# Performance work log

Measured on AMD Instinct MI355X. Metric: run time of the kernel, lower is better.

The kernel has to match this reference:

```python
import jax, jax.numpy as jnp
import numpy as np

ALPHA = 0.2          # LeakyReLU negative slope
ORTHO_LAMBDA = 0.01  # orthogonal regularization weight


def setup_inputs() -> dict:
    key = jax.random.key(0)
    ks = jax.random.split(key, 9)
    N, IN, OUT, NR, H = 50000, 128, 128, 64, 4
    E1, E2 = 200000, 50000
    return {
        "input": jax.random.normal(ks[0], (N, IN), jnp.float32),
        "edge": jax.random.randint(ks[1], (2, E1), 0, N),
        "edge_embed": jax.random.normal(ks[2], (E1, NR), jnp.float32),
        "edge_list_nhop": jax.random.randint(ks[3], (2, E2), 0, N),
        "edge_embed_nhop": jax.random.normal(ks[4], (E2, NR), jnp.float32),
        "proj": jax.random.normal(ks[5], (H, IN, IN), jnp.float32) / np.sqrt(IN).astype(np.float32),
        "W": jax.random.normal(ks[6], (H, OUT, 2 * IN + NR), jnp.float32) * 0.08,
        "a": jax.random.normal(ks[7], (H, 1, OUT), jnp.float32) * 0.1,
        "head_weights": jnp.ones((H,), jnp.float32),
    }


def reference(input, edge, edge_embed, edge_list_nhop, edge_embed_nhop, proj, W, a, head_weights):
    N, IN = input.shape
    H, OUT, _ = W.shape
    e = jnp.concatenate([edge, edge_list_nhop], axis=1)              # [2, E]
    emb = jnp.concatenate([edge_embed, edge_embed_nhop], axis=0)     # [E, NR]
    src, tgt = e[0], e[1]

    # per-head orthogonal projections: head_input[h] = input @ proj[h].T -> [H, N, IN]
    hin = jnp.einsum('ni,hoi->hno', input, proj)

    # edge_m = W @ concat(h_src, h_tgt, rel) without materializing the concat
    W_src, W_tgt, W_rel = W[:, :, :IN], W[:, :, IN:2 * IN], W[:, :, 2 * IN:]
    edge_m = (jnp.einsum('hei,hoi->heo', hin[:, src, :], W_src)
              + jnp.einsum('hei,hoi->heo', hin[:, tgt, :], W_tgt)
              + jnp.einsum('er,hor->heo', emb, W_rel))               # [H, E, OUT]

    scores = jnp.einsum('heo,ho->he', edge_m, a[:, 0, :])            # [H, E]
    powers = -jnp.where(scores > 0, scores, ALPHA * scores)         # -leakyrelu
    edge_e = jnp.exp(powers)                                         # [H, E]

    seg = lambda v: jax.ops.segment_sum(v, src, num_segments=N)
    e_rowsum = jnp.clip(jax.vmap(seg)(edge_e), 1e-12, None)          # [H, N]

    edge_w = edge_e[:, :, None] * edge_m                             # [H, E, OUT]
    head_out = jax.vmap(seg)(edge_w)                                 # [H, N, OUT]

    w = jax.nn.softmax(head_weights)
    out = jnp.einsum('h,hnd->nd', w, head_out)                       # [N, OUT]
    # faithful to torch: divides by the LAST head's e_rowsum (loop leakage)
    out = out / e_rowsum[-1][:, None]

    pp = jnp.einsum('hij,hkj->hik', proj, proj)                      # proj @ proj.T
    eye = jnp.eye(proj.shape[1], dtype=proj.dtype)
    orth_reg = ORTHO_LAMBDA * jnp.sum(jnp.sqrt(jnp.sum((pp - eye) ** 2, axis=(1, 2))))

    return jax.nn.elu(out), orth_reg
```

## Files before the change

### kernel.cpp

```cpp
#include <hip/hip_runtime.h>
#include <math.h>


#define NHEAD 4

typedef unsigned short u16;
typedef __attribute__((ext_vector_type(4))) unsigned short u16x4;
typedef __attribute__((ext_vector_type(8))) unsigned short u16x8;
typedef __attribute__((ext_vector_type(8))) short bf16x8;
typedef __attribute__((ext_vector_type(4))) float f32x4;

__device__ __forceinline__ float bf2f(u16 v) {
    union { unsigned u; float f; } x; x.u = ((unsigned)v) << 16; return x.f;
}
__device__ __forceinline__ u16 f2bf(float f) {
    union { float f; unsigned u; } x; x.f = f;
    const unsigned r = x.u + 0x7FFFu + ((x.u >> 16) & 1u);
    return (u16)(r >> 16);
}

__global__ __launch_bounds__(256) void k1_prep(
    const float* __restrict__ proj, const float* __restrict__ W,
    const float* __restrict__ a, const float* __restrict__ hw,
    u16* __restrict__ M_bf,
    float* __restrict__ asrc, float* __restrict__ atgt, float* __restrict__ arel,
    u16* __restrict__ WcatT_bf, float* __restrict__ wsoft,
    float* __restrict__ orth_part)
{
    __shared__ float projS[128*132];
    __shared__ float WS[32*132];
    __shared__ float tS[128];
    __shared__ float red[256];
    const int h = blockIdx.x;
    const int part = blockIdx.y;
    const int z = blockIdx.z;
    const int tid = threadIdx.x;
    if (part < 2 && z >= 4) return;
    const float* projH = proj + h*(128*128);
    const float* WH = W + h*(128*320);
    const float* aH = a + h*128;

    {
        const float4* p4 = (const float4*)projH;
        for (int idx = tid; idx < 4096; idx += 256)
            *(float4*)&projS[(idx>>5)*132 + (idx&31)*4] = p4[idx];
    }

    if (part < 2) {
        const int koff = part ? 128 : 0;
        for (int idx = tid; idx < 1024; idx += 256) {
            const int ol = idx>>5, jq = idx&31;
            *(float4*)&WS[ol*132 + jq*4] = *(const float4*)&WH[(z*32+ol)*320 + koff + jq*4];
        }
        __syncthreads();
        u16* Mout = M_bf + ((size_t)(part*4 + h))*16384;
        for (int idx = tid; idx < 1024; idx += 256) {
            const int ol = idx>>5, jq = idx&31;
            float4 acc; acc.x=0.f; acc.y=0.f; acc.z=0.f; acc.w=0.f;
            for (int i = 0; i < 128; ++i) {
                const float wv = WS[ol*132 + i];
                const float4 pv = *(const float4*)&projS[i*132 + jq*4];
                acc.x += wv*pv.x; acc.y += wv*pv.y; acc.z += wv*pv.z; acc.w += wv*pv.w;
            }
            u16x4 pk; pk.x=f2bf(acc.x); pk.y=f2bf(acc.y); pk.z=f2bf(acc.z); pk.w=f2bf(acc.w);
            *(u16x4*)&Mout[(z*32+ol)*128 + jq*4] = pk;
        }
        if (z == 0) {
            if (tid < 128) {
                float s = 0.f;
                for (int o = 0; o < 128; ++o) s += aH[o]*WH[o*320 + koff + tid];
                tS[tid] = s;
            }
            __syncthreads();
            if (tid < 128) {
                float s = 0.f;
                for (int i = 0; i < 128; ++i) s += tS[i]*projS[i*132 + tid];
                (part ? atgt : asrc)[h*128 + tid] = s;
            }
        }
    } else {
        __syncthreads();
        float local = 0.f;
        const int base = z*2048;
        for (int idx = base + tid; idx < base + 2048; idx += 256) {
            const int i = idx>>7, k = idx&127;
            if (i > k) continue;
            float s = 0.f;
            for (int q = 0; q < 32; ++q) {
                const float4 pi = *(const float4*)&projS[i*132 + q*4];
                const float4 pk = *(const float4*)&projS[k*132 + q*4];
                s += pi.x*pk.x + pi.y*pk.y + pi.z*pk.z + pi.w*pk.w;
            }
            if (i == k) { s -= 1.f; local += s*s; }
            else local += 2.f*s*s;
        }
        red[tid] = local;
        __syncthreads();
        for (int st = 128; st > 0; st >>= 1) {
            if (tid < st) red[tid] += red[tid+st];
            __syncthreads();
        }
        if (tid == 0) atomicAdd(&orth_part[h], red[0]);
        if (z == 0) {
            if (tid < 64) {
                float s = 0.f;
                for (int o = 0; o < 128; ++o) s += aH[o]*WH[o*320 + 256 + tid];
                arel[h*64 + tid] = s;
            }
            for (int idx = tid; idx < 8192; idx += 256) {
                const int r = idx & 63, o = idx >> 6;
                WcatT_bf[(size_t)o*256 + h*64 + r] = f2bf(WH[o*320 + 256 + r]);
            }
            if (h == 0 && tid == 0) {
                const float m = fmaxf(fmaxf(hw[0],hw[1]), fmaxf(hw[2],hw[3]));
                const float e0=expf(hw[0]-m), e1=expf(hw[1]-m), e2=expf(hw[2]-m), e3=expf(hw[3]-m);
                const float s = e0+e1+e2+e3;
                wsoft[0]=e0/s; wsoft[1]=e1/s; wsoft[2]=e2/s; wsoft[3]=e3/s;
            }
        }
    }
}

__global__ __launch_bounds__(256) void k0_nodes(
    const float* __restrict__ input, const float* __restrict__ asrc, const float* __restrict__ atgt,
    u16* __restrict__ in_bf, float* __restrict__ s_src, float* __restrict__ s_tgt, int N)
{
    __shared__ float aS[512], tS[512];
    const int tid = threadIdx.x;
    for (int idx = tid; idx < 512; idx += 256) { aS[idx] = asrc[idx]; tS[idx] = atgt[idx]; }
    __syncthreads();
    const int n = blockIdx.x*256 + tid;
    if (n >= N) return;
    const float4* inr = (const float4*)(input + (size_t)n*128);
    u16* ob = in_bf + (size_t)n*128;
    float ss[4] = {0.f,0.f,0.f,0.f}, st[4] = {0.f,0.f,0.f,0.f};
    for (int q = 0; q < 32; ++q) {
        const float4 v = inr[q];
        u16x4 pk; pk.x=f2bf(v.x); pk.y=f2bf(v.y); pk.z=f2bf(v.z); pk.w=f2bf(v.w);
        *(u16x4*)(ob + q*4) = pk;
        #pragma unroll
        for (int hh = 0; hh < 4; ++hh) {
            const float4 av = *(const float4*)&aS[hh*128 + q*4];
            const float4 tv = *(const float4*)&tS[hh*128 + q*4];
            ss[hh] += v.x*av.x + v.y*av.y + v.z*av.z + v.w*av.w;
            st[hh] += v.x*tv.x + v.y*tv.y + v.z*tv.z + v.w*tv.w;
        }
    }
    float4 o1; o1.x=ss[0]; o1.y=ss[1]; o1.z=ss[2]; o1.w=ss[3];
    float4 o2; o2.x=st[0]; o2.y=st[1]; o2.z=st[2]; o2.w=st[3];
    *(float4*)(s_src + (size_t)n*4) = o1;
    *(float4*)(s_tgt + (size_t)n*4) = o2;
}

__global__ __launch_bounds__(256) void k2_mfma(
    const u16* __restrict__ in_bf, const u16* __restrict__ M_bf,
    u16* __restrict__ tbl, int N)
{
    __shared__ u16 MS[16384];
    __shared__ u16 DW[4][16*136];
    const int tid = threadIdx.x;
    const int w = tid >> 6, lane = tid & 63;
    const int bid = blockIdx.x;
    const int nx = gridDim.x >> 3;
    const int swz = (bid & 7)*nx + (bid >> 3);
    const int n0 = (swz >> 3)*256;
    const int mat = swz & 7;
    const int m = lane & 15, kg = lane >> 4;

    {
        const u16* Mp = M_bf + (size_t)mat*16384;
        for (int c = tid; c < 2048; c += 256) {
            const int row = c >> 4, c16 = c & 15;
            const u16x8 v = *(const u16x8*)(Mp + row*128 + c16*8);
            *(u16x8*)((char*)MS + row*256 + ((c16*16) ^ ((row&7)<<4))) = v;
        }
    }
    __syncthreads();

    bf16x8 fa[8][4];
    #pragma unroll
    for (int nt = 0; nt < 8; ++nt) {
        const int row = nt*16 + m;
        #pragma unroll
        for (int ks = 0; ks < 4; ++ks) {
            const int c16 = ks*4 + kg;
            fa[nt][ks] = *(const bf16x8*)((const char*)MS + row*256 + ((c16*16) ^ ((row&7)<<4)));
        }
    }

    for (int sub = 0; sub < 4; ++sub) {
        const int nrow = n0 + w*64 + sub*16 + m;
        const int nclamp = (nrow < N) ? nrow : (N-1);
        bf16x8 fb[4];
        #pragma unroll
        for (int ks = 0; ks < 4; ++ks)
            fb[ks] = *(const bf16x8*)(in_bf + (size_t)nclamp*128 + ks*32 + kg*8);
        f32x4 acc[8];
        #pragma unroll
        for (int nt = 0; nt < 8; ++nt) { acc[nt][0]=0.f; acc[nt][1]=0.f; acc[nt][2]=0.f; acc[nt][3]=0.f; }
        #pragma unroll
        for (int nt = 0; nt < 8; ++nt)
            #pragma unroll
            for (int ks = 0; ks < 4; ++ks)
                acc[nt] = __builtin_amdgcn_mfma_f32_16x16x32_bf16(fa[nt][ks], fb[ks], acc[nt], 0, 0, 0);
        #pragma unroll
        for (int nt = 0; nt < 8; ++nt) {
            unsigned lo, hi;
            asm("v_cvt_pk_bf16_f32 %0, %1, %2" : "=v"(lo) : "v"(acc[nt][0]), "v"(acc[nt][1]));
            asm("v_cvt_pk_bf16_f32 %0, %1, %2" : "=v"(hi) : "v"(acc[nt][2]), "v"(acc[nt][3]));
            uint2 pk; pk.x = lo; pk.y = hi;
            *(uint2*)&DW[w][m*136 + nt*16 + kg*4] = pk;
        }
        __syncthreads();
        const int nb = n0 + w*64 + sub*16;
        #pragma unroll
        for (int k = 0; k < 4; ++k) {
            const int idx = lane + k*64;
            const int row = idx >> 4, seg = idx & 15;
            const int n = nb + row;
            if (n < N) {
                const bf16x8 v = *(const bf16x8*)&DW[w][row*136 + seg*8];
                *(bf16x8*)(tbl + (size_t)n*1024 + mat*128 + seg*8) = v;
            }
        }
        __syncthreads();
    }
}

__global__ __launch_bounds__(256) void k_deg(
    const int* __restrict__ edge, const int* __restrict__ nhop,
    int* __restrict__ deg, int E1, int E2)
{
    const int e = blockIdx.x*256 + threadIdx.x;
    if (e >= E1+E2) return;
    const int src = (e < E1) ? edge[e] : nhop[e-E1];
    atomicAdd(&deg[src], 1);
}

__global__ __launch_bounds__(1024) void k_scanA(const int* __restrict__ deg, int* __restrict__ offsets,
                                                int* __restrict__ bsum, int N)
{
    __shared__ int wsumS[16];
    const int tid = threadIdx.x;
    const int lane = tid & 63, wid = tid >> 6;
    const int i0 = blockIdx.x*4096 + tid*4;
    int a0=0,a1=0,a2=0,a3=0;
    if (i0 + 3 < N) { const int4 t = *(const int4*)(deg + i0); a0=t.x; a1=t.y; a2=t.z; a3=t.w; }
    else { if (i0 < N) a0=deg[i0]; if (i0+1 < N) a1=deg[i0+1]; if (i0+2 < N) a2=deg[i0+2]; }
    const int s1=a0+a1, s2=s1+a2, s3=s2+a3;
    int s = s3;
    #pragma unroll
    for (int d = 1; d < 64; d <<= 1) { const int t = __shfl_up(s, d); if (lane >= d) s += t; }
    if (lane == 63) wsumS[wid] = s;
    __syncthreads();
    if (tid < 16) {
        int t = wsumS[tid];
        #pragma unroll
        for (int d = 1; d < 16; d <<= 1) { const int u = __shfl_up(t, d); if (tid >= d) t += u; }
        wsumS[tid] = t;
    }
    __syncthreads();
    const int ex = (wid ? wsumS[wid-1] : 0) + s - s3;
    if (i0 < N)     offsets[i0]   = ex;
    if (i0+1 < N)   offsets[i0+1] = ex + a0;
    if (i0+2 < N)   offsets[i0+2] = ex + s1;
    if (i0+3 < N)   offsets[i0+3] = ex + s2;
    if (tid == 0) bsum[blockIdx.x] = wsumS[15];
}

__global__ __launch_bounds__(64) void k_scanB(const int* __restrict__ bsum, int* __restrict__ boff,
                                              int* __restrict__ offsets, int nb, int N)
{
    const int tid = threadIdx.x;
    const int v = (tid < nb) ? bsum[tid] : 0;
    int s = v;
    #pragma unroll
    for (int d = 1; d < 64; d <<= 1) { const int t = __shfl_up(s, d); if (tid >= d) s += t; }
    if (tid < nb) boff[tid] = s - v;
    if (tid == 63) offsets[N] = s;
}

__global__ __launch_bounds__(256) void k_fill2(
    const int* __restrict__ edge, const int* __restrict__ nhop,
    const float* __restrict__ emb1, const float* __restrict__ emb2,
    const float* __restrict__ s_src, const float* __restrict__ s_tgt,
    const float* __restrict__ arel,
    const int* __restrict__ offsets, const int* __restrict__ boff, int* __restrict__ cursor,
    int* __restrict__ csr_tgt, float* __restrict__ ee_perm, u16* __restrict__ emb_perm,
    int E1, int E2)
{
    const int tid = threadIdx.x;
    const int g = tid >> 4, l = tid & 15;
    const int E = E1 + E2;
    const float4 ar0 = *(const float4*)(arel + 0*64 + l*4);
    const float4 ar1 = *(const float4*)(arel + 1*64 + l*4);
    const float4 ar2 = *(const float4*)(arel + 2*64 + l*4);
    const float4 ar3 = *(const float4*)(arel + 3*64 + l*4);
    const int ebase = blockIdx.x*256;
    #pragma unroll 4
    for (int it = 0; it < 16; ++it) {
        const int e = ebase + it*16 + g;
        if (e >= E) continue;
        const float4 v = (e < E1) ? *(const float4*)(emb1 + (size_t)e*64 + l*4)
                                  : *(const float4*)(emb2 + (size_t)(e-E1)*64 + l*4);
        u16x4 pk; pk.x=f2bf(v.x); pk.y=f2bf(v.y); pk.z=f2bf(v.z); pk.w=f2bf(v.w);
        float p0 = v.x*ar0.x + v.y*ar0.y + v.z*ar0.z + v.w*ar0.w;
        float p1 = v.x*ar1.x + v.y*ar1.y + v.z*ar1.z + v.w*ar1.w;
        float p2 = v.x*ar2.x + v.y*ar2.y + v.z*ar2.z + v.w*ar2.w;
        float p3 = v.x*ar3.x + v.y*ar3.y + v.z*ar3.z + v.w*ar3.w;
        #pragma unroll
        for (int d = 1; d < 16; d <<= 1) {
            p0 += __shfl_xor(p0, d);
            p1 += __shfl_xor(p1, d);
            p2 += __shfl_xor(p2, d);
            p3 += __shfl_xor(p3, d);
        }
        int p = 0;
        if (l == 0) {
            int src, tgt;
            if (e < E1) { src = edge[e]; tgt = edge[E1+e]; }
            else { const int e2 = e-E1; src = nhop[e2]; tgt = nhop[E2+e2]; }
            const float4 s4 = *(const float4*)(s_src + (size_t)src*4);
            const float4 t4 = *(const float4*)(s_tgt + (size_t)tgt*4);
            float4 eo;
            { const float sc = s4.x+t4.x+p0; eo.x = expf(sc>0.f ? -sc : -0.2f*sc); }
            { const float sc = s4.y+t4.y+p1; eo.y = expf(sc>0.f ? -sc : -0.2f*sc); }
            { const float sc = s4.z+t4.z+p2; eo.z = expf(sc>0.f ? -sc : -0.2f*sc); }
            { const float sc = s4.w+t4.w+p3; eo.w = expf(sc>0.f ? -sc : -0.2f*sc); }
            const int pos = atomicAdd(&cursor[src], 1);
            p = offsets[src] + boff[src>>12] + pos;
            csr_tgt[p] = tgt;
            *(float4*)(ee_perm + (size_t)p*4) = eo;
        }
        p = __shfl(p, tid & 48);
        *(u16x4*)(emb_perm + (size_t)p*64 + l*4) = pk;
    }
}

__global__ __launch_bounds__(256) void k4_gather(
    const float* __restrict__ ee_perm, const int* __restrict__ offsets, const int* __restrict__ boff,
    const int* __restrict__ csr_tgt,
    const u16* __restrict__ emb_perm, const u16* __restrict__ tbl,
    const float* __restrict__ wsoft,
    u16* __restrict__ pout_bf, u16* __restrict__ semb_bf, float* __restrict__ rowsum3,
    int N)
{
    __shared__ float eeS[4][64][4];
    __shared__ int   tgS[4][64];
    const int lane = threadIdx.x & 63;
    const int wv = threadIdx.x >> 6;
    const int n = blockIdx.x*4 + wv;
    if (n >= N) return;
    const int hl = lane >> 4;
    const int hoff = hl*128 + (lane & 15)*8;

    union HT { u16x8 v; unsigned u[4]; };

    float acc[8];
    #pragma unroll
    for (int j = 0; j < 8; ++j) acc[j] = 0.f;
    float sm0=0.f, sm1=0.f, sm2=0.f, sm3=0.f;
    float rsl0=0.f, rsl1=0.f, rsl2=0.f, rsl3=0.f;

    const int start = offsets[n] + boff[n>>12];
    const int end = (n+1 == N) ? offsets[N] : (offsets[n+1] + boff[(n+1)>>12]);
    for (int cb = start; cb < end; cb += 64) {
        const int rem = end - cb;
        const int cnt = rem < 64 ? rem : 64;
        int tgtL = 0;
        float4 eeL; eeL.x=0.f; eeL.y=0.f; eeL.z=0.f; eeL.w=0.f;
        if (lane < cnt) {
            tgtL = csr_tgt[cb + lane];
            eeL  = *(const float4*)(ee_perm + (size_t)(cb + lane)*4);
        }
        rsl0 += eeL.x; rsl1 += eeL.y; rsl2 += eeL.z; rsl3 += eeL.w;
        *(float4*)&eeS[wv][lane][0] = eeL;
        tgS[wv][lane] = tgtL;
        const int cp = (cnt + 3) & ~3;

        HT zz; zz.u[0]=0u; zz.u[1]=0u; zz.u[2]=0u; zz.u[3]=0u;
        HT ht0=zz, ht1=zz, ht2=zz, ht3=zz;
        u16 em0=0, em1=0, em2=0, em3=0;
#define K4_FETCH(J, IDX) { const int tg_ = tgS[wv][IDX]; \
            ht##J.v = *(const u16x8*)(tbl + (size_t)tg_*1024 + 512 + hoff); \
            em##J = emb_perm[(size_t)(cb + (IDX))*64 + lane]; }
        if (0 < cnt) K4_FETCH(0, 0)
        if (1 < cnt) K4_FETCH(1, 1)
        if (2 < cnt) K4_FETCH(2, 2)
        if (3 < cnt) K4_FETCH(3, 3)

#define K4_STAGE(J) { \
            const float4 ee4 = *(const float4*)&eeS[wv][i+J][0]; \
            const float eh = eeS[wv][i+J][hl]; \
            _Pragma("unroll") \
            for (int p = 0; p < 4; ++p) { \
                union{unsigned u; float f;} lo_, hi_; \
                lo_.u = ht##J.u[p] << 16; hi_.u = ht##J.u[p] & 0xffff0000u; \
                acc[2*p]   += eh*lo_.f; \
                acc[2*p+1] += eh*hi_.f; \
            } \
            const float ev = bf2f(em##J); \
            sm0 += ee4.x*ev; sm1 += ee4.y*ev; sm2 += ee4.z*ev; sm3 += ee4.w*ev; \
            { const int ii = i + 4 + J; if (ii < cnt) K4_FETCH(J, ii) } }

        for (int i = 0; i < cp; i += 4) {
            K4_STAGE(0)
            K4_STAGE(1)
            K4_STAGE(2)
            K4_STAGE(3)
        }
#undef K4_STAGE
#undef K4_FETCH
    }

    #pragma unroll
    for (int d = 1; d < 64; d <<= 1) {
        rsl0 += __shfl_xor(rsl0, d);
        rsl1 += __shfl_xor(rsl1, d);
        rsl2 += __shfl_xor(rsl2, d);
        rsl3 += __shfl_xor(rsl3, d);
    }
    {
        const float rsh = (hl==0)?rsl0:(hl==1)?rsl1:(hl==2)?rsl2:rsl3;
        HT hs; hs.v = *(const u16x8*)(tbl + (size_t)n*1024 + hoff);
        #pragma unroll
        for (int p = 0; p < 4; ++p) {
            union{unsigned u; float f;} lo_, hi_;
            lo_.u = hs.u[p] << 16; hi_.u = hs.u[p] & 0xffff0000u;
            acc[2*p]   += rsh*lo_.f;
            acc[2*p+1] += rsh*hi_.f;
        }
    }
    if (lane == 0) rowsum3[n] = fmaxf(rsl3, 1e-12f);

    const float4 ws4 = *(const float4*)wsoft;
    const float wh = (hl==0)?ws4.x:(hl==1)?ws4.y:(hl==2)?ws4.z:ws4.w;
    float p[8];
    #pragma unroll
    for (int j = 0; j < 8; ++j) {
        float pv = wh*acc[j];
        pv += __shfl_xor(pv, 16);
        pv += __shfl_xor(pv, 32);
        p[j] = pv;
    }
    if (hl == 0) {
        u16 pk[8];
        #pragma unroll
        for (int j = 0; j < 8; ++j) pk[j] = f2bf(p[j]);
        *(u16x8*)(pout_bf + (size_t)n*128 + (lane & 15)*8) = *(u16x8*)pk;
    }
    u16* so = semb_bf + (size_t)n*256;
    so[lane]       = f2bf(ws4.x*sm0);
    so[64 + lane]  = f2bf(ws4.y*sm1);
    so[128 + lane] = f2bf(ws4.z*sm2);
    so[192 + lane] = f2bf(ws4.w*sm3);
}

__global__ __launch_bounds__(256) void k5_gemm(
    const u16* __restrict__ semb_bf, const u16* __restrict__ wcatT_bf,
    const u16* __restrict__ pout_bf,
    const float* __restrict__ rowsum3, const float* __restrict__ orth_part,
    float* __restrict__ out, int N)
{
    __shared__ float DS[64*132];
    const int tid = threadIdx.x;
    if (blockIdx.x == 0 && tid == 0)
        out[(size_t)N*128] = 0.01f*(sqrtf(orth_part[0])+sqrtf(orth_part[1])+sqrtf(orth_part[2])+sqrtf(orth_part[3]));
    const int w = tid >> 6, lane = tid & 63;
    const int m = lane & 15, kg = lane >> 4;
    const int n0 = blockIdx.x*64;

    bf16x8 fa[8];
    {
        int row = n0 + w*16 + m; if (row >= N) row = N-1;
        const u16* ap = semb_bf + (size_t)row*256 + kg*8;
        #pragma unroll
        for (int ks = 0; ks < 8; ++ks) fa[ks] = *(const bf16x8*)(ap + ks*32);
    }
    f32x4 acc[8];
    #pragma unroll
    for (int nt = 0; nt < 8; ++nt) { acc[nt][0]=0.f; acc[nt][1]=0.f; acc[nt][2]=0.f; acc[nt][3]=0.f; }
    #pragma unroll
    for (int nt = 0; nt < 8; ++nt) {
        const u16* bp = wcatT_bf + (size_t)(nt*16 + m)*256 + kg*8;
        #pragma unroll
        for (int ks = 0; ks < 8; ++ks) {
            const bf16x8 fb = *(const bf16x8*)(bp + ks*32);
            acc[nt] = __builtin_amdgcn_mfma_f32_16x16x32_bf16(fa[ks], fb, acc[nt], 0, 0, 0);
        }
    }
    #pragma unroll
    for (int nt = 0; nt < 8; ++nt) {
        const int o = nt*16 + m;
        const int r0 = w*16 + kg*4;
        #pragma unroll
        for (int r = 0; r < 4; ++r)
            DS[(r0+r)*132 + o] = acc[nt][r];
    }
    __syncthreads();
    for (int idx = tid; idx < 2048; idx += 256) {
        const int row = idx >> 5, q = idx & 31;
        const int n = n0 + row;
        if (n < N) {
            const float4 d = *(const float4*)&DS[row*132 + q*4];
            const u16x4 pb = *(const u16x4*)(pout_bf + (size_t)n*128 + q*4);
            const float rinv = 1.0f / rowsum3[n];
            float v0 = (bf2f(pb.x) + d.x)*rinv;
            float v1 = (bf2f(pb.y) + d.y)*rinv;
            float v2 = (bf2f(pb.z) + d.z)*rinv;
            float v3 = (bf2f(pb.w) + d.w)*rinv;
            v0 = (v0 > 0.f) ? v0 : expm1f(v0);
            v1 = (v1 > 0.f) ? v1 : expm1f(v1);
            v2 = (v2 > 0.f) ? v2 : expm1f(v2);
            v3 = (v3 > 0.f) ? v3 : expm1f(v3);
            float4 r4; r4.x=v0; r4.y=v1; r4.z=v2; r4.w=v3;
            *(float4*)(out + (size_t)n*128 + q*4) = r4;
        }
    }
}

extern "C" void kernel_launch(void* const* d_in, const int* in_sizes, int n_in,
                              void* d_out, int out_size, void* d_ws, size_t ws_size,
                              hipStream_t stream)
{
    const float* input = (const float*)d_in[0];
    const int*   edge  = (const int*)d_in[1];
    const float* emb1  = (const float*)d_in[2];
    const int*   nhop  = (const int*)d_in[3];
    const float* emb2  = (const float*)d_in[4];
    const float* proj  = (const float*)d_in[5];
    const float* W     = (const float*)d_in[6];
    const float* a     = (const float*)d_in[7];
    const float* hw    = (const float*)d_in[8];
    float* out = (float*)d_out;

    const int N  = in_sizes[0] / 128;
    const int E1 = in_sizes[1] / 2;
    const int E2 = in_sizes[3] / 2;
    const int E  = E1 + E2;
    (void)n_in; (void)out_size; (void)ws_size;

    char* wsb = (char*)d_ws;
    size_t off = 0;
    auto alloc = [&](size_t bytes) -> char* {
        char* p = wsb + off;
        off += (bytes + 255) & ~(size_t)255;
        return p;
    };
    u16*   in_bf    = (u16*)alloc((size_t)N*128*2);
    u16*   tbl      = (u16*)alloc((size_t)N*1024*2);
    u16*   semb_bf  = (u16*)alloc((size_t)N*256*2);
    u16*   pout_bf  = (u16*)alloc((size_t)N*128*2);
    u16*   emb_perm = (u16*)alloc((size_t)E*64*2);
    float* ee_perm  = (float*)alloc((size_t)E*4*4);
    int*   csr_tgt  = (int*)alloc((size_t)E*4);
    u16*   M_bf     = (u16*)alloc((size_t)8*16384*2);
    u16*   WcatT_bf = (u16*)alloc((size_t)128*256*2);
    float* asrc     = (float*)alloc(512*4);
    float* atgt     = (float*)alloc(512*4);
    float* arel     = (float*)alloc(256*4);
    float* s_src    = (float*)alloc((size_t)N*4*4);
    float* s_tgt    = (float*)alloc((size_t)N*4*4);
    float* wsoft    = (float*)alloc(4*4);
    float* rowsum3  = (float*)alloc((size_t)N*4);
    int*   offsets  = (int*)alloc((size_t)(N+1)*4);
    int*   bsum     = (int*)alloc(64*4);
    int*   boff     = (int*)alloc(64*4);
    const size_t zoff0 = off;
    float* orth_part= (float*)alloc(4*4);
    int*   deg      = (int*)alloc((size_t)N*4);
    int*   cursor   = (int*)alloc((size_t)N*4);
    const size_t zoff1 = off;

    hipMemsetAsync(wsb + zoff0, 0, zoff1 - zoff0, stream);

    const int nbScan = (N + 4095) / 4096;
    const int nx = (N + 255) / 256;

    k1_prep<<<dim3(NHEAD,3,8), dim3(256), 0, stream>>>(proj, W, a, hw, M_bf,
                                                       asrc, atgt, arel, WcatT_bf, wsoft, orth_part);
    k0_nodes<<<dim3((N+255)/256), dim3(256), 0, stream>>>(input, asrc, atgt, in_bf, s_src, s_tgt, N);
    k2_mfma<<<dim3(nx*8), dim3(256), 0, stream>>>(in_bf, M_bf, tbl, N);
    k_deg<<<dim3((E+255)/256), dim3(256), 0, stream>>>(edge, nhop, deg, E1, E2);
    k_scanA<<<dim3(nbScan), dim3(1024), 0, stream>>>(deg, offsets, bsum, N);
    k_scanB<<<dim3(1), dim3(64), 0, stream>>>(bsum, boff, offsets, nbScan, N);
    k_fill2<<<dim3((E+255)/256), dim3(256), 0, stream>>>(edge, nhop, emb1, emb2, s_src, s_tgt,
                                                         arel, offsets, boff, cursor,
                                                         csr_tgt, ee_perm, emb_perm, E1, E2);
    k4_gather<<<dim3((N+3)/4), dim3(256), 0, stream>>>(ee_perm, offsets, boff, csr_tgt, emb_perm,
                                                       tbl, wsoft, pout_bf, semb_bf, rowsum3, N);
    k5_gemm<<<dim3((N+63)/64), dim3(256), 0, stream>>>(semb_bf, WcatT_bf, pout_bf, rowsum3, orth_part,
                                                       out, N);
}
```

Measured before the change: 257.6 us.

## Fuse degree count into node prep and co-schedule edge fill with MFMA table GEMM

Moves the per-edge degree atomics into the node-prep kernel, extending its grid to cover all edges. Merges the edge-fill kernel and the projection-table MFMA kernel into one launch whose blocks branch by index, so the independent fill and GEMM work can overlap. It also removes the block barriers around the per-wave staging buffer in the GEMM path. This cuts launches and idle tails, at the cost of the fill blocks now carrying the GEMM's large shared-memory allocation, which may lower their occupancy.

```diff
diff --git a/kernel.cpp b/kernel.cpp
--- a/kernel.cpp
+++ b/kernel.cpp
@@ -123,13 +123,20 @@
 
 __global__ __launch_bounds__(256) void k0_nodes(
     const float* __restrict__ input, const float* __restrict__ asrc, const float* __restrict__ atgt,
-    u16* __restrict__ in_bf, float* __restrict__ s_src, float* __restrict__ s_tgt, int N)
+    const int* __restrict__ edge, const int* __restrict__ nhop,
+    u16* __restrict__ in_bf, float* __restrict__ s_src, float* __restrict__ s_tgt,
+    int* __restrict__ deg, int N, int E1, int E2)
 {
     __shared__ float aS[512], tS[512];
     const int tid = threadIdx.x;
     for (int idx = tid; idx < 512; idx += 256) { aS[idx] = asrc[idx]; tS[idx] = atgt[idx]; }
+    const int t = blockIdx.x*256 + tid;
+    if (t < E1 + E2) {
+        const int src = (t < E1) ? edge[t] : nhop[t-E1];
+        atomicAdd(&deg[src], 1);
+    }
     __syncthreads();
-    const int n = blockIdx.x*256 + tid;
+    const int n = t;
     if (n >= N) return;
     const float4* inr = (const float4*)(input + (size_t)n*128);
     u16* ob = in_bf + (size_t)n*128;
@@ -150,91 +157,6 @@
     float4 o2; o2.x=st[0]; o2.y=st[1]; o2.z=st[2]; o2.w=st[3];
     *(float4*)(s_src + (size_t)n*4) = o1;
     *(float4*)(s_tgt + (size_t)n*4) = o2;
-}
-
-__global__ __launch_bounds__(256) void k2_mfma(
-    const u16* __restrict__ in_bf, const u16* __restrict__ M_bf,
-    u16* __restrict__ tbl, int N)
-{
-    __shared__ u16 MS[16384];
-    __shared__ u16 DW[4][16*136];
-    const int tid = threadIdx.x;
-    const int w = tid >> 6, lane = tid & 63;
-    const int bid = blockIdx.x;
-    const int nx = gridDim.x >> 3;
-    const int swz = (bid & 7)*nx + (bid >> 3);
-    const int n0 = (swz >> 3)*256;
-    const int mat = swz & 7;
-    const int m = lane & 15, kg = lane >> 4;
-
-    {
-        const u16* Mp = M_bf + (size_t)mat*16384;
-        for (int c = tid; c < 2048; c += 256) {
-            const int row = c >> 4, c16 = c & 15;
-            const u16x8 v = *(const u16x8*)(Mp + row*128 + c16*8);
-            *(u16x8*)((char*)MS + row*256 + ((c16*16) ^ ((row&7)<<4))) = v;
-        }
-    }
-    __syncthreads();
-
-    bf16x8 fa[8][4];
-    #pragma unroll
-    for (int nt = 0; nt < 8; ++nt) {
-        const int row = nt*16 + m;
-        #pragma unroll
-        for (int ks = 0; ks < 4; ++ks) {
-            const int c16 = ks*4 + kg;
-            fa[nt][ks] = *(const bf16x8*)((const char*)MS + row*256 + ((c16*16) ^ ((row&7)<<4)));
-        }
-    }
-
-    for (int sub = 0; sub < 4; ++sub) {
-        const int nrow = n0 + w*64 + sub*16 + m;
-        const int nclamp = (nrow < N) ? nrow : (N-1);
-        bf16x8 fb[4];
-        #pragma unroll
-        for (int ks = 0; ks < 4; ++ks)
-            fb[ks] = *(const bf16x8*)(in_bf + (size_t)nclamp*128 + ks*32 + kg*8);
-        f32x4 acc[8];
-        #pragma unroll
-        for (int nt = 0; nt < 8; ++nt) { acc[nt][0]=0.f; acc[nt][1]=0.f; acc[nt][2]=0.f; acc[nt][3]=0.f; }
-        #pragma unroll
-        for (int nt = 0; nt < 8; ++nt)
-            #pragma unroll
-            for (int ks = 0; ks < 4; ++ks)
-                acc[nt] = __builtin_amdgcn_mfma_f32_16x16x32_bf16(fa[nt][ks], fb[ks], acc[nt], 0, 0, 0);
-        #pragma unroll
-        for (int nt = 0; nt < 8; ++nt) {
-            unsigned lo, hi;
-            asm("v_cvt_pk_bf16_f32 %0, %1, %2" : "=v"(lo) : "v"(acc[nt][0]), "v"(acc[nt][1]));
-            asm("v_cvt_pk_bf16_f32 %0, %1, %2" : "=v"(hi) : "v"(acc[nt][2]), "v"(acc[nt][3]));
-            uint2 pk; pk.x = lo; pk.y = hi;
-            *(uint2*)&DW[w][m*136 + nt*16 + kg*4] = pk;
-        }
-        __syncthreads();
-        const int nb = n0 + w*64 + sub*16;
-        #pragma unroll
-        for (int k = 0; k < 4; ++k) {
-            const int idx = lane + k*64;
-            const int row = idx >> 4, seg = idx & 15;
-            const int n = nb + row;
-            if (n < N) {
-                const bf16x8 v = *(const bf16x8*)&DW[w][row*136 + seg*8];
-                *(bf16x8*)(tbl + (size_t)n*1024 + mat*128 + seg*8) = v;
-            }
-        }
-        __syncthreads();
-    }
-}
-
-__global__ __launch_bounds__(256) void k_deg(
-    const int* __restrict__ edge, const int* __restrict__ nhop,
-    int* __restrict__ deg, int E1, int E2)
-{
-    const int e = blockIdx.x*256 + threadIdx.x;
-    if (e >= E1+E2) return;
-    const int src = (e < E1) ? edge[e] : nhop[e-E1];
-    atomicAdd(&deg[src], 1);
 }
 
 __global__ __launch_bounds__(1024) void k_scanA(const int* __restrict__ deg, int* __restrict__ offsets,
@@ -280,60 +202,133 @@
     if (tid == 63) offsets[N] = s;
 }
 
-__global__ __launch_bounds__(256) void k_fill2(
+__global__ __launch_bounds__(256) void kC_fill_gemm(
     const int* __restrict__ edge, const int* __restrict__ nhop,
     const float* __restrict__ emb1, const float* __restrict__ emb2,
     const float* __restrict__ s_src, const float* __restrict__ s_tgt,
     const float* __restrict__ arel,
     const int* __restrict__ offsets, const int* __restrict__ boff, int* __restrict__ cursor,
     int* __restrict__ csr_tgt, float* __restrict__ ee_perm, u16* __restrict__ emb_perm,
-    int E1, int E2)
-{
+    int E1, int E2, int nfill,
+    const u16* __restrict__ in_bf, const u16* __restrict__ M_bf,
+    u16* __restrict__ tbl, int N, int nx8)
+{
+    __shared__ u16 MS[16384];
+    __shared__ u16 DW[4][16*136];
     const int tid = threadIdx.x;
-    const int g = tid >> 4, l = tid & 15;
-    const int E = E1 + E2;
-    const float4 ar0 = *(const float4*)(arel + 0*64 + l*4);
-    const float4 ar1 = *(const float4*)(arel + 1*64 + l*4);
-    const float4 ar2 = *(const float4*)(arel + 2*64 + l*4);
-    const float4 ar3 = *(const float4*)(arel + 3*64 + l*4);
-    const int ebase = blockIdx.x*256;
-    #pragma unroll 4
-    for (int it = 0; it < 16; ++it) {
-        const int e = ebase + it*16 + g;
-        if (e >= E) continue;
-        const float4 v = (e < E1) ? *(const float4*)(emb1 + (size_t)e*64 + l*4)
-                                  : *(const float4*)(emb2 + (size_t)(e-E1)*64 + l*4);
-        u16x4 pk; pk.x=f2bf(v.x); pk.y=f2bf(v.y); pk.z=f2bf(v.z); pk.w=f2bf(v.w);
-        float p0 = v.x*ar0.x + v.y*ar0.y + v.z*ar0.z + v.w*ar0.w;
-        float p1 = v.x*ar1.x + v.y*ar1.y + v.z*ar1.z + v.w*ar1.w;
-        float p2 = v.x*ar2.x + v.y*ar2.y + v.z*ar2.z + v.w*ar2.w;
-        float p3 = v.x*ar3.x + v.y*ar3.y + v.z*ar3.z + v.w*ar3.w;
-        #pragma unroll
-        for (int d = 1; d < 16; d <<= 1) {
-            p0 += __shfl_xor(p0, d);
-            p1 += __shfl_xor(p1, d);
-            p2 += __shfl_xor(p2, d);
-            p3 += __shfl_xor(p3, d);
-        }
-        int p = 0;
-        if (l == 0) {
-            int src, tgt;
-            if (e < E1) { src = edge[e]; tgt = edge[E1+e]; }
-            else { const int e2 = e-E1; src = nhop[e2]; tgt = nhop[E2+e2]; }
-            const float4 s4 = *(const float4*)(s_src + (size_t)src*4);
-            const float4 t4 = *(const float4*)(s_tgt + (size_t)tgt*4);
-            float4 eo;
-            { const float sc = s4.x+t4.x+p0; eo.x = expf(sc>0.f ? -sc : -0.2f*sc); }
-            { const float sc = s4.y+t4.y+p1; eo.y = expf(sc>0.f ? -sc : -0.2f*sc); }
-            { const float sc = s4.z+t4.z+p2; eo.z = expf(sc>0.f ? -sc : -0.2f*sc); }
-            { const float sc = s4.w+t4.w+p3; eo.w = expf(sc>0.f ? -sc : -0.2f*sc); }
-            const int pos = atomicAdd(&cursor[src], 1);
-            p = offsets[src] + boff[src>>12] + pos;
-            csr_tgt[p] = tgt;
-            *(float4*)(ee_perm + (size_t)p*4) = eo;
-        }
-        p = __shfl(p, tid & 48);
-        *(u16x4*)(emb_perm + (size_t)p*64 + l*4) = pk;
+
+    if (blockIdx.x < nfill) {
+        const int g = tid >> 4, l = tid & 15;
+        const int E = E1 + E2;
+        const float4 ar0 = *(const float4*)(arel + 0*64 + l*4);
+        const float4 ar1 = *(const float4*)(arel + 1*64 + l*4);
+        const float4 ar2 = *(const float4*)(arel + 2*64 + l*4);
+        const float4 ar3 = *(const float4*)(arel + 3*64 + l*4);
+        const int ebase = blockIdx.x*256;
+        #pragma unroll 4
+        for (int it = 0; it < 16; ++it) {
+            const int e = ebase + it*16 + g;
+            if (e >= E) continue;
+            const float4 v = (e < E1) ? *(const float4*)(emb1 + (size_t)e*64 + l*4)
+                                      : *(const float4*)(emb2 + (size_t)(e-E1)*64 + l*4);
+            u16x4 pk; pk.x=f2bf(v.x); pk.y=f2bf(v.y); pk.z=f2bf(v.z); pk.w=f2bf(v.w);
+            float p0 = v.x*ar0.x + v.y*ar0.y + v.z*ar0.z + v.w*ar0.w;
+            float p1 = v.x*ar1.x + v.y*ar1.y + v.z*ar1.z + v.w*ar1.w;
+            float p2 = v.x*ar2.x + v.y*ar2.y + v.z*ar2.z + v.w*ar2.w;
+            float p3 = v.x*ar3.x + v.y*ar3.y + v.z*ar3.z + v.w*ar3.w;
+            #pragma unroll
+            for (int d = 1; d < 16; d <<= 1) {
+                p0 += __shfl_xor(p0, d);
+                p1 += __shfl_xor(p1, d);
+                p2 += __shfl_xor(p2, d);
+                p3 += __shfl_xor(p3, d);
+            }
+            int p = 0;
+            if (l == 0) {
+                int src, tgt;
+                if (e < E1) { src = edge[e]; tgt = edge[E1+e]; }
+                else { const int e2 = e-E1; src = nhop[e2]; tgt = nhop[E2+e2]; }
+                const float4 s4 = *(const float4*)(s_src + (size_t)src*4);
+                const float4 t4 = *(const float4*)(s_tgt + (size_t)tgt*4);
+                float4 eo;
+                { const float sc = s4.x+t4.x+p0; eo.x = expf(sc>0.f ? -sc : -0.2f*sc); }
+                { const float sc = s4.y+t4.y+p1; eo.y = expf(sc>0.f ? -sc : -0.2f*sc); }
+                { const float sc = s4.z+t4.z+p2; eo.z = expf(sc>0.f ? -sc : -0.2f*sc); }
+                { const float sc = s4.w+t4.w+p3; eo.w = expf(sc>0.f ? -sc : -0.2f*sc); }
+                const int pos = atomicAdd(&cursor[src], 1);
+                p = offsets[src] + boff[src>>12] + pos;
+                csr_tgt[p] = tgt;
+                *(float4*)(ee_perm + (size_t)p*4) = eo;
+            }
+            p = __shfl(p, tid & 48);
+            *(u16x4*)(emb_perm + (size_t)p*64 + l*4) = pk;
+        }
+        return;
+    }
+
+    const int bid = blockIdx.x - nfill;
+    const int w = tid >> 6, lane = tid & 63;
+    const int nx = nx8 >> 3;
+    const int swz = (bid & 7)*nx + (bid >> 3);
+    const int n0 = (swz >> 3)*256;
+    const int mat = swz & 7;
+    const int m = lane & 15, kg = lane >> 4;
+
+    {
+        const u16* Mp = M_bf + (size_t)mat*16384;
+        for (int c = tid; c < 2048; c += 256) {
+            const int row = c >> 4, c16 = c & 15;
+            const u16x8 v = *(const u16x8*)(Mp + row*128 + c16*8);
+            *(u16x8*)((char*)MS + row*256 + ((c16*16) ^ ((row&7)<<4))) = v;
+        }
+    }
+    __syncthreads();
+
+    bf16x8 fa[8][4];
+    #pragma unroll
+    for (int nt = 0; nt < 8; ++nt) {
+        const int row = nt*16 + m;
+        #pragma unroll
+        for (int ks = 0; ks < 4; ++ks) {
+            const int c16 = ks*4 + kg;
+            fa[nt][ks] = *(const bf16x8*)((const char*)MS + row*256 + ((c16*16) ^ ((row&7)<<4)));
+        }
+    }
+
+    for (int sub = 0; sub < 4; ++sub) {
+        const int nrow = n0 + w*64 + sub*16 + m;
+        const int nclamp = (nrow < N) ? nrow : (N-1);
+        bf16x8 fb[4];
+        #pragma unroll
+        for (int ks = 0; ks < 4; ++ks)
+            fb[ks] = *(const bf16x8*)(in_bf + (size_t)nclamp*128 + ks*32 + kg*8);
+        f32x4 acc[8];
+        #pragma unroll
+        for (int nt = 0; nt < 8; ++nt) { acc[nt][0]=0.f; acc[nt][1]=0.f; acc[nt][2]=0.f; acc[nt][3]=0.f; }
+        #pragma unroll
+        for (int nt = 0; nt < 8; ++nt)
+            #pragma unroll
+            for (int ks = 0; ks < 4; ++ks)
+                acc[nt] = __builtin_amdgcn_mfma_f32_16x16x32_bf16(fa[nt][ks], fb[ks], acc[nt], 0, 0, 0);
+        #pragma unroll
+        for (int nt = 0; nt < 8; ++nt) {
+            unsigned lo, hi;
+            asm("v_cvt_pk_bf16_f32 %0, %1, %2" : "=v"(lo) : "v"(acc[nt][0]), "v"(acc[nt][1]));
+            asm("v_cvt_pk_bf16_f32 %0, %1, %2" : "=v"(hi) : "v"(acc[nt][2]), "v"(acc[nt][3]));
+            uint2 pk; pk.x = lo; pk.y = hi;
+            *(uint2*)&DW[w][m*136 + nt*16 + kg*4] = pk;
+        }
+        const int nb = n0 + w*64 + sub*16;
+        #pragma unroll
+        for (int k = 0; k < 4; ++k) {
+            const int idx = lane + k*64;
+            const int row = idx >> 4, seg = idx & 15;
+            const int n = nb + row;
+            if (n < N) {
+                const bf16x8 v = *(const bf16x8*)&DW[w][row*136 + seg*8];
+                *(bf16x8*)(tbl + (size_t)n*1024 + mat*128 + seg*8) = v;
+            }
+        }
     }
 }
 
@@ -576,17 +571,20 @@
 
     const int nbScan = (N + 4095) / 4096;
     const int nx = (N + 255) / 256;
+    const int nx8 = nx*8;
+    const int nfill = (E + 255) / 256;
+    const int nk0 = ((E > N ? E : N) + 255) / 256;
 
     k1_prep<<<dim3(NHEAD,3,8), dim3(256), 0, stream>>>(proj, W, a, hw, M_bf,
                                                        asrc, atgt, arel, WcatT_bf, wsoft, orth_part);
-    k0_nodes<<<dim3((N+255)/256), dim3(256), 0, stream>>>(input, asrc, atgt, in_bf, s_src, s_tgt, N);
-    k2_mfma<<<dim3(nx*8), dim3(256), 0, stream>>>(in_bf, M_bf, tbl, N);
-    k_deg<<<dim3((E+255)/256), dim3(256), 0, stream>>>(edge, nhop, deg, E1, E2);
+    k0_nodes<<<dim3(nk0), dim3(256), 0, stream>>>(input, asrc, atgt, edge, nhop,
+                                                  in_bf, s_src, s_tgt, deg, N, E1, E2);
     k_scanA<<<dim3(nbScan), dim3(1024), 0, stream>>>(deg, offsets, bsum, N);
     k_scanB<<<dim3(1), dim3(64), 0, stream>>>(bsum, boff, offsets, nbScan, N);
-    k_fill2<<<dim3((E+255)/256), dim3(256), 0, stream>>>(edge, nhop, emb1, emb2, s_src, s_tgt,
-                                                         arel, offsets, boff, cursor,
-                                                         csr_tgt, ee_perm, emb_perm, E1, E2);
+    kC_fill_gemm<<<dim3(nfill + nx8), dim3(256), 0, stream>>>(
+        edge, nhop, emb1, emb2, s_src, s_tgt, arel, offsets, boff, cursor,
+        csr_tgt, ee_perm, emb_perm, E1, E2, nfill,
+        in_bf, M_bf, tbl, N, nx8);
     k4_gather<<<dim3((N+3)/4), dim3(256), 0, stream>>>(ee_perm, offsets, boff, csr_tgt, emb_perm,
                                                        tbl, wsoft, pout_bf, semb_bf, rowsum3, N);
     k5_gemm<<<dim3((N+63)/64), dim3(256), 0, stream>>>(semb_bf, WcatT_bf, pout_bf, rowsum3, orth_part,
```

After: 265.0 us. +2.8%, slower.

## Fuse degree count into node kernel, merge scan passes, drop k2 barriers

Applied to the files above, without the earlier changes.

Folds the edge-degree atomic counting into the node preprocessing kernel, which now launches enough blocks to cover both edges and nodes. The two-pass scan is merged into one kernel, where the last block to finish (found with an atomic ticket) scans the block sums. Two __syncthreads in the MFMA table kernel are removed. The aim is fewer kernel launches and less barrier overhead. Without those barriers, a wave may read LDS rows written by other lanes without synchronisation, which risks a race unless each wave only touches its own DW slice.

```diff
diff --git a/kernel.cpp b/kernel.cpp
--- a/kernel.cpp
+++ b/kernel.cpp
@@ -123,13 +123,20 @@
 
 __global__ __launch_bounds__(256) void k0_nodes(
     const float* __restrict__ input, const float* __restrict__ asrc, const float* __restrict__ atgt,
-    u16* __restrict__ in_bf, float* __restrict__ s_src, float* __restrict__ s_tgt, int N)
+    const int* __restrict__ edge, const int* __restrict__ nhop,
+    u16* __restrict__ in_bf, float* __restrict__ s_src, float* __restrict__ s_tgt,
+    int* __restrict__ deg, int N, int E1, int E2)
 {
     __shared__ float aS[512], tS[512];
     const int tid = threadIdx.x;
     for (int idx = tid; idx < 512; idx += 256) { aS[idx] = asrc[idx]; tS[idx] = atgt[idx]; }
+    const int t = blockIdx.x*256 + tid;
+    if (t < E1 + E2) {
+        const int src = (t < E1) ? edge[t] : nhop[t-E1];
+        atomicAdd(&deg[src], 1);
+    }
     __syncthreads();
-    const int n = blockIdx.x*256 + tid;
+    const int n = t;
     if (n >= N) return;
     const float4* inr = (const float4*)(input + (size_t)n*128);
     u16* ob = in_bf + (size_t)n*128;
@@ -211,7 +218,6 @@
             uint2 pk; pk.x = lo; pk.y = hi;
             *(uint2*)&DW[w][m*136 + nt*16 + kg*4] = pk;
         }
-        __syncthreads();
         const int nb = n0 + w*64 + sub*16;
         #pragma unroll
         for (int k = 0; k < 4; ++k) {
@@ -223,24 +229,15 @@
                 *(bf16x8*)(tbl + (size_t)n*1024 + mat*128 + seg*8) = v;
             }
         }
-        __syncthreads();
-    }
-}
-
-__global__ __launch_bounds__(256) void k_deg(
-    const int* __restrict__ edge, const int* __restrict__ nhop,
-    int* __restrict__ deg, int E1, int E2)
-{
-    const int e = blockIdx.x*256 + threadIdx.x;
-    if (e >= E1+E2) return;
-    const int src = (e < E1) ? edge[e] : nhop[e-E1];
-    atomicAdd(&deg[src], 1);
+    }
 }
 
 __global__ __launch_bounds__(1024) void k_scanA(const int* __restrict__ deg, int* __restrict__ offsets,
-                                                int* __restrict__ bsum, int N)
+                                                int* __restrict__ bsum, int* __restrict__ boff,
+                                                int* __restrict__ sdone, int N, int nb)
 {
     __shared__ int wsumS[16];
+    __shared__ int ticketS;
     const int tid = threadIdx.x;
     const int lane = tid & 63, wid = tid >> 6;
     const int i0 = blockIdx.x*4096 + tid*4;
@@ -265,19 +262,20 @@
     if (i0+1 < N)   offsets[i0+1] = ex + a0;
     if (i0+2 < N)   offsets[i0+2] = ex + s1;
     if (i0+3 < N)   offsets[i0+3] = ex + s2;
-    if (tid == 0) bsum[blockIdx.x] = wsumS[15];
-}
-
-__global__ __launch_bounds__(64) void k_scanB(const int* __restrict__ bsum, int* __restrict__ boff,
-                                              int* __restrict__ offsets, int nb, int N)
-{
-    const int tid = threadIdx.x;
-    const int v = (tid < nb) ? bsum[tid] : 0;
-    int s = v;
-    #pragma unroll
-    for (int d = 1; d < 64; d <<= 1) { const int t = __shfl_up(s, d); if (tid >= d) s += t; }
-    if (tid < nb) boff[tid] = s - v;
-    if (tid == 63) offsets[N] = s;
+    if (tid == 0) {
+        bsum[blockIdx.x] = wsumS[15];
+        __threadfence();
+        ticketS = atomicAdd(sdone, 1);
+    }
+    __syncthreads();
+    if (ticketS == nb - 1 && tid < 64) {
+        const int v = (tid < nb) ? atomicAdd(&bsum[tid], 0) : 0;
+        int sv = v;
+        #pragma unroll
+        for (int d = 1; d < 64; d <<= 1) { const int t = __shfl_up(sv, d); if (tid >= d) sv += t; }
+        if (tid < nb) boff[tid] = sv - v;
+        if (tid == 63) offsets[N] = sv;
+    }
 }
 
 __global__ __launch_bounds__(256) void k_fill2(
@@ -570,20 +568,21 @@
     float* orth_part= (float*)alloc(4*4);
     int*   deg      = (int*)alloc((size_t)N*4);
     int*   cursor   = (int*)alloc((size_t)N*4);
+    int*   sdone    = (int*)alloc(4);
     const size_t zoff1 = off;
 
     hipMemsetAsync(wsb + zoff0, 0, zoff1 - zoff0, stream);
 
     const int nbScan = (N + 4095) / 4096;
     const int nx = (N + 255) / 256;
+    const int nk0 = ((E > N ? E : N) + 255) / 256;
 
     k1_prep<<<dim3(NHEAD,3,8), dim3(256), 0, stream>>>(proj, W, a, hw, M_bf,
                                                        asrc, atgt, arel, WcatT_bf, wsoft, orth_part);
-    k0_nodes<<<dim3((N+255)/256), dim3(256), 0, stream>>>(input, asrc, atgt, in_bf, s_src, s_tgt, N);
+    k0_nodes<<<dim3(nk0), dim3(256), 0, stream>>>(input, asrc, atgt, edge, nhop,
+                                                  in_bf, s_src, s_tgt, deg, N, E1, E2);
     k2_mfma<<<dim3(nx*8), dim3(256), 0, stream>>>(in_bf, M_bf, tbl, N);
-    k_deg<<<dim3((E+255)/256), dim3(256), 0, stream>>>(edge, nhop, deg, E1, E2);
-    k_scanA<<<dim3(nbScan), dim3(1024), 0, stream>>>(deg, offsets, bsum, N);
-    k_scanB<<<dim3(1), dim3(64), 0, stream>>>(bsum, boff, offsets, nbScan, N);
+    k_scanA<<<dim3(nbScan), dim3(1024), 0, stream>>>(deg, offsets, bsum, boff, sdone, N, nbScan);
     k_fill2<<<dim3((E+255)/256), dim3(256), 0, stream>>>(edge, nhop, emb1, emb2, s_src, s_tgt,
                                                          arel, offsets, boff, cursor,
                                                          csr_tgt, ee_perm, emb_perm, E1, E2);
```

Result: faster. 248.9 us (-3.4%).
